# Performance work log

Measured on AMD Instinct MI355X. Metric: run time of the kernel, lower is better.

Reference implementation:

```python
import jax, jax.numpy as jnp
import numpy as np

N_NODES = 50000
N_EDGES = 1600000
IN_CH = 128
HID = 128
OUT_CH = 6
NUM_GRAPHS = 512


def _lin_params(key, fan_in, fan_out):
    k1, k2 = jax.random.split(key)
    bound = 1.0 / np.sqrt(fan_in)
    W = jax.random.uniform(k1, (fan_in, fan_out), minval=-bound, maxval=bound, dtype=jnp.float32)
    b = jax.random.uniform(k2, (fan_out,), minval=-bound, maxval=bound, dtype=jnp.float32)
    return W, b


def setup_inputs() -> dict:
    key = jax.random.key(0)
    ks = jax.random.split(key, 10)
    x = jax.random.normal(ks[0], (N_NODES, IN_CH), dtype=jnp.float32)
    edge_index = jax.random.randint(ks[1], (2, N_EDGES), 0, N_NODES, dtype=jnp.int64)
    batch = jnp.sort(jax.random.randint(ks[2], (N_NODES,), 0, NUM_GRAPHS, dtype=jnp.int64))
    W1a, b1a = _lin_params(ks[3], IN_CH, HID)
    W1b, b1b = _lin_params(ks[4], HID, HID)
    W2a, b2a = _lin_params(ks[5], HID, HID)
    W2b, b2b = _lin_params(ks[6], HID, HID)
    Wf1, bf1 = _lin_params(ks[7], HID, HID)
    Wf2, bf2 = _lin_params(ks[8], HID, OUT_CH)
    return {"x": x, "edge_index": edge_index, "batch": batch,
            "W1a": W1a, "b1a": b1a, "W1b": W1b, "b1b": b1b,
            "W2a": W2a, "b2a": b2a, "W2b": W2b, "b2b": b2b,
            "Wf1": Wf1, "bf1": bf1, "Wf2": Wf2, "bf2": bf2}


def _gin_conv(x, src, dst, Wa, ba, Wb, bb):
    # aggregate: sum of source-node features into target nodes (eps = 0)
    agg = jax.ops.segment_sum(x[src], dst, num_segments=N_NODES)
    h = x + agg  # (1 + eps) * x + sum_neighbors
    h = jax.nn.relu(h @ Wa + ba) @ Wb + bb  # 2-layer MLP (nn1/nn2)
    return h


def reference(x, edge_index, batch, W1a, b1a, W1b, b1b, W2a, b2a, W2b, b2b, Wf1, bf1, Wf2, bf2):
    src, dst = edge_index[0], edge_index[1]
    h = jax.nn.relu(_gin_conv(x, src, dst, W1a, b1a, W1b, b1b))
    h = jax.nn.relu(_gin_conv(h, src, dst, W2a, b2a, W2b, b2b))
    # global mean pool over graph ids
    sums = jax.ops.segment_sum(h, batch, num_segments=NUM_GRAPHS)  # [G, HID]
    counts = jax.ops.segment_sum(jnp.ones((h.shape[0],), h.dtype), batch, num_segments=NUM_GRAPHS)
    pooled = sums / jnp.maximum(counts, 1.0)[:, None]
    out = jax.nn.relu(pooled @ Wf1 + bf1) @ Wf2 + bf2  # [G, 6]
    return jax.nn.sigmoid(out)
```

## Files before the change

kernel.cpp:

```cpp
#include <hip/hip_runtime.h>

typedef unsigned short u16;
typedef unsigned int u32;

#define N_NODES 50000
#define N_EDGES 1600000
#define CH 128
#define CHW 64
#define NG 512
#define CAP 128
#define PAD 136
#define NBINS 196
#define BINCAP 12288
#define ECHUNK 6250

typedef __bf16 bf16x8 __attribute__((ext_vector_type(8)));
typedef float f32x4 __attribute__((ext_vector_type(4)));

#define OFF_DEG 0ull
#define OFF_BUCKET 200192ull
#define OFF_XB 13000192ull
#define OFF_HSUM 25800192ull
#define OFF_H1 38600192ull
#define OFF_POOL 51400192ull
#define OFF_GS 51662336ull
#define OFF_GE 51664384ull
#define OFF_WT 51666432ull
#define OFF_BC 51797504ull
#define OFF_WF1 51799552ull
#define OFF_BF1 51865088ull
#define OFF_WF2 51865600ull
#define OFF_BF2 51868672ull
#define OFF_BCUR 51868928ull

__device__ __forceinline__ float bflo(u32 v) { return __builtin_bit_cast(float, v << 16); }
__device__ __forceinline__ float bfhi(u32 v) { return __builtin_bit_cast(float, v & 0xffff0000u); }
__device__ __forceinline__ float bf2f(u16 v) { return __builtin_bit_cast(float, ((u32)v) << 16); }
__device__ __forceinline__ u16 f2bf(float f) {
    u32 x = __builtin_bit_cast(u32, f);
    x += 0x7fffu + ((x >> 16) & 1u);
    return (u16)(x >> 16);
}
__device__ __forceinline__ u32 pack2(float a, float b) {
    return (u32)f2bf(a) | ((u32)f2bf(b) << 16);
}
__device__ __forceinline__ bool probe_bf16(u32 w0) {
    u32 ex = (w0 >> 7) & 0xFFu;
    bool ok = ((w0 & 0x7FFFu) == 0u) || (ex >= 0x70u && ex <= 0x8Fu);
    return __popcll(__ballot(ok)) >= 48;
}
__device__ __forceinline__ float loadf(const void* p, int i, bool isbf) {
    return isbf ? bf2f(((const u16*)p)[i]) : ((const float*)p)[i];
}

__global__ __launch_bounds__(256) void prep_params(char* ws,
                                                   const void* W0, const void* W1,
                                                   const void* W2, const void* W3,
                                                   const void* b0, const void* b1,
                                                   const void* b2, const void* b3,
                                                   const void* Wf1, const void* bf1,
                                                   const void* Wf2, const void* bf2) {
    int lane = threadIdx.x & 63;
    bool isbf = probe_bf16(((const u32*)W0)[lane]);
    int idx = blockIdx.x * 256 + threadIdx.x;
    u16* Wt = (u16*)(ws + OFF_WT);
    float* bc = (float*)(ws + OFF_BC);
    float* Wf1c = (float*)(ws + OFF_WF1);
    float* bf1c = (float*)(ws + OFF_BF1);
    float* Wf2c = (float*)(ws + OFF_WF2);
    float* bf2c = (float*)(ws + OFF_BF2);
    if (idx < 65536) {
        int j = idx >> 14, r = idx & 16383;
        int n = r >> 7, k = r & 127;
        const void* src = (j == 0) ? W0 : (j == 1) ? W1 : (j == 2) ? W2 : W3;
        float v = loadf(src, k * 128 + n, isbf);
        Wt[idx] = f2bf(v);
    } else if (idx < 66048) {
        int r = idx - 65536, j = r >> 7, c = r & 127;
        const void* src = (j == 0) ? b0 : (j == 1) ? b1 : (j == 2) ? b2 : b3;
        bc[r] = loadf(src, c, isbf);
    } else if (idx < 82432) {
        Wf1c[idx - 66048] = loadf(Wf1, idx - 66048, isbf);
    } else if (idx < 82560) {
        bf1c[idx - 82432] = loadf(bf1, idx - 82432, isbf);
    } else if (idx < 83328) {
        Wf2c[idx - 82560] = loadf(Wf2, idx - 82560, isbf);
    } else if (idx < 83334) {
        bf2c[idx - 83328] = loadf(bf2, idx - 83328, isbf);
    }
}

__global__ __launch_bounds__(256) void cvt_x(const u32* __restrict__ x, u32* __restrict__ xb) {
    int lane = threadIdx.x & 63;
    bool isbf = probe_bf16(x[lane]);
    int i = blockIdx.x * 256 + threadIdx.x;
    if (i >= N_NODES * CHW) return;
    if (isbf) {
        xb[i] = x[i];
    } else {
        float2 v = ((const float2*)x)[i];
        xb[i] = pack2(v.x, v.y);
    }
}

__global__ __launch_bounds__(256) void edge_scatter(const int* __restrict__ ei,
                                                    int* __restrict__ binCursor,
                                                    u32* __restrict__ binned) {
    __shared__ u32 lhist[256];
    __shared__ u32 lbase[256];
    __shared__ u32 lcur[256];
    int tid = threadIdx.x, wg = blockIdx.x;
    int lane = tid & 63;
    u32 hiw = ((const u32*)ei)[2 * lane + 1];
    bool i64 = __popcll(__ballot(hiw == 0u)) >= 48;
    int e0 = wg * ECHUNK;
    lhist[tid] = 0; lcur[tid] = 0;
    __syncthreads();
    for (int e = e0 + tid; e < e0 + ECHUNK; e += 256) {
        int d = i64 ? ei[2 * N_EDGES + 2 * e] : ei[N_EDGES + e];
        atomicAdd(&lhist[d >> 8], 1u);
    }
    __syncthreads();
    u32 c = lhist[tid];
    if (c) lbase[tid] = (u32)atomicAdd(&binCursor[tid], (int)c);
    __syncthreads();
    for (int e = e0 + tid; e < e0 + ECHUNK; e += 256) {
        int s, d;
        if (i64) { s = ei[2 * e]; d = ei[2 * N_EDGES + 2 * e]; }
        else     { s = ei[e];     d = ei[N_EDGES + e]; }
        int b = d >> 8;
        u32 p = atomicAdd(&lcur[b], 1u);
        binned[(size_t)b * BINCAP + lbase[b] + p] = ((u32)d << 16) | (u32)s;
    }
}

__global__ __launch_bounds__(256) void fill_from_binned(const int* __restrict__ binCursor,
                                                        const u32* __restrict__ binned,
                                                        int* __restrict__ deg,
                                                        u16* __restrict__ bucket) {
    __shared__ u32 ldeg[256];
    int tid = threadIdx.x, b = blockIdx.x;
    int cnt = binCursor[b];
    ldeg[tid] = 0;
    __syncthreads();
    const u32* bp = binned + (size_t)b * BINCAP;
    for (int i = tid; i < cnt; i += 256) {
        u32 w = bp[i];
        u32 dl = (w >> 16) & 255u;
        u32 pos = atomicAdd(&ldeg[dl], 1u);
        if (pos < CAP) bucket[(size_t)(w >> 16) * CAP + pos] = (u16)(w & 0xFFFFu);
    }
    __syncthreads();
    int node = b * 256 + tid;
    if (node < N_NODES) deg[node] = (int)ldeg[tid];
}

__global__ __launch_bounds__(256) void agg_kernel(const u32* __restrict__ h,
                                                  const int* __restrict__ deg,
                                                  const u16* __restrict__ bucket,
                                                  u32* __restrict__ out) {
    int w = threadIdx.x >> 6, lane = threadIdx.x & 63;
    int node = blockIdx.x * 4 + w;
    if (node >= N_NODES) return;
    u32 self = h[(size_t)node * CHW + lane];
    float ax = bflo(self), ay = bfhi(self);
    int d = deg[node];
    d = d > CAP ? CAP : d;
    const u16* bk = bucket + (size_t)node * CAP;
    const u32* bkw = (const u32*)bk;
    int j = 0;
    for (; j + 8 <= d; j += 8) {
        u32 w0 = bkw[(j >> 1) + 0], w1 = bkw[(j >> 1) + 1];
        u32 w2 = bkw[(j >> 1) + 2], w3 = bkw[(j >> 1) + 3];
        u32 v0 = h[(size_t)(w0 & 0xFFFFu) * CHW + lane];
        u32 v1 = h[(size_t)(w0 >> 16) * CHW + lane];
        u32 v2 = h[(size_t)(w1 & 0xFFFFu) * CHW + lane];
        u32 v3 = h[(size_t)(w1 >> 16) * CHW + lane];
        u32 v4 = h[(size_t)(w2 & 0xFFFFu) * CHW + lane];
        u32 v5 = h[(size_t)(w2 >> 16) * CHW + lane];
        u32 v6 = h[(size_t)(w3 & 0xFFFFu) * CHW + lane];
        u32 v7 = h[(size_t)(w3 >> 16) * CHW + lane];
        ax += bflo(v0) + bflo(v1) + bflo(v2) + bflo(v3)
            + bflo(v4) + bflo(v5) + bflo(v6) + bflo(v7);
        ay += bfhi(v0) + bfhi(v1) + bfhi(v2) + bfhi(v3)
            + bfhi(v4) + bfhi(v5) + bfhi(v6) + bfhi(v7);
    }
    for (; j < d; ++j) {
        u32 v = h[(size_t)bk[j] * CHW + lane];
        ax += bflo(v);
        ay += bfhi(v);
    }
    out[(size_t)node * CHW + lane] = pack2(ax, ay);
}

__global__ __launch_bounds__(256) void mlp_kernel(const u16* __restrict__ in,
                                                  const u16* __restrict__ Wta,
                                                  const float* __restrict__ ba,
                                                  const u16* __restrict__ Wtb,
                                                  const float* __restrict__ bb,
                                                  u16* __restrict__ out,
                                                  int nrows) {
    __shared__ __align__(16) u16 Wlds[128 * PAD];
    __shared__ __align__(16) u16 tlds[64 * PAD];
    const int tid = threadIdx.x;
    const int w = tid >> 6;
    const int lane = tid & 63;
    const int n16 = lane & 15;
    const int quad = lane >> 4;
    const int row0 = blockIdx.x * 64 + w * 16;
    const bool active = row0 < nrows;

    {
        const uint4* wsrc = (const uint4*)Wta;
#pragma unroll
        for (int it = 0; it < 8; ++it) {
            int idx = tid + it * 256;
            int n = idx >> 4, c = idx & 15;
            *(uint4*)&Wlds[n * PAD + c * 8] = wsrc[idx];
        }
    }
    __syncthreads();

    f32x4 acc[8];
    bf16x8 afrag[4];
    if (active) {
        const u16* rowp = in + (size_t)(row0 + n16) * CH + quad * 8;
#pragma unroll
        for (int ks = 0; ks < 4; ++ks)
            afrag[ks] = *(const bf16x8*)(rowp + ks * 32);
#pragma unroll
        for (int ct = 0; ct < 8; ++ct) {
            f32x4 a = {0.f, 0.f, 0.f, 0.f};
#pragma unroll
            for (int ks = 0; ks < 4; ++ks) {
                bf16x8 b = *(const bf16x8*)&Wlds[(u32)(ct * 16 + n16) * PAD + ks * 32 + quad * 8];
                a = __builtin_amdgcn_mfma_f32_16x16x32_bf16(afrag[ks], b, a, 0, 0, 0);
            }
            acc[ct] = a;
        }
#pragma unroll
        for (int ct = 0; ct < 8; ++ct) {
            float bv = ba[ct * 16 + n16];
#pragma unroll
            for (int r = 0; r < 4; ++r) {
                float v = fmaxf(acc[ct][r] + bv, 0.f);
                tlds[(w * 16 + quad * 4 + r) * PAD + ct * 16 + n16] = f2bf(v);
            }
        }
    }
    __syncthreads();
    {
        const uint4* wsrc = (const uint4*)Wtb;
#pragma unroll
        for (int it = 0; it < 8; ++it) {
            int idx = tid + it * 256;
            int n = idx >> 4, c = idx & 15;
            *(uint4*)&Wlds[n * PAD + c * 8] = wsrc[idx];
        }
    }
    __syncthreads();

    if (active) {
#pragma unroll
        for (int ks = 0; ks < 4; ++ks)
            afrag[ks] = *(const bf16x8*)&tlds[(u32)(w * 16 + n16) * PAD + ks * 32 + quad * 8];
#pragma unroll
        for (int ct = 0; ct < 8; ++ct) {
            f32x4 a = {0.f, 0.f, 0.f, 0.f};
#pragma unroll
            for (int ks = 0; ks < 4; ++ks) {
                bf16x8 b = *(const bf16x8*)&Wlds[(u32)(ct * 16 + n16) * PAD + ks * 32 + quad * 8];
                a = __builtin_amdgcn_mfma_f32_16x16x32_bf16(afrag[ks], b, a, 0, 0, 0);
            }
            acc[ct] = a;
        }
#pragma unroll
        for (int ct = 0; ct < 8; ++ct) {
            float bv = bb[ct * 16 + n16];
#pragma unroll
            for (int r = 0; r < 4; ++r) {
                float v = fmaxf(acc[ct][r] + bv, 0.f);
                tlds[(w * 16 + quad * 4 + r) * PAD + ct * 16 + n16] = f2bf(v);
            }
        }
        u32* outw = (u32*)out;
        for (int r = 0; r < 16; ++r) {
            u32 v = *(const u32*)&tlds[(w * 16 + r) * PAD + lane * 2];
            outw[(size_t)(row0 + r) * CHW + lane] = v;
        }
    }
}

__global__ __launch_bounds__(256) void graph_bounds(const int* __restrict__ batch,
                                                    int* __restrict__ gstart,
                                                    int* __restrict__ gend) {
    int lane = threadIdx.x & 63;
    u32 hiw = ((const u32*)batch)[2 * (12500 + lane) + 1];
    bool i64 = __popcll(__ballot(hiw == 0u)) >= 48;
    int i = blockIdx.x * 256 + threadIdx.x;
    if (i >= N_NODES) return;
    int g = i64 ? batch[2 * i] : batch[i];
    atomicMin(&gstart[g], i);
    atomicMax(&gend[g], i + 1);
}

__global__ __launch_bounds__(256) void pool_kernel(const u32* __restrict__ h,
                                                   const int* __restrict__ gstart,
                                                   const int* __restrict__ gend,
                                                   float* __restrict__ pooled) {
    int w = threadIdx.x >> 6, lane = threadIdx.x & 63;
    int g = blockIdx.x * 4 + w;
    if (g >= NG) return;
    int s = gstart[g], e = gend[g];
    float ax = 0.f, ay = 0.f;
    if (s < e) {
        int i = s;
        for (; i + 4 <= e; i += 4) {
            u32 v0 = h[(size_t)(i + 0) * CHW + lane];
            u32 v1 = h[(size_t)(i + 1) * CHW + lane];
            u32 v2 = h[(size_t)(i + 2) * CHW + lane];
            u32 v3 = h[(size_t)(i + 3) * CHW + lane];
            ax += bflo(v0) + bflo(v1) + bflo(v2) + bflo(v3);
            ay += bfhi(v0) + bfhi(v1) + bfhi(v2) + bfhi(v3);
        }
        for (; i < e; ++i) {
            u32 v = h[(size_t)i * CHW + lane];
            ax += bflo(v);
            ay += bfhi(v);
        }
    }
    float inv = 1.f / (float)((s < e) ? (e - s) : 1);
    ((float2*)pooled)[(size_t)g * CHW + lane] = make_float2(ax * inv, ay * inv);
}

__global__ __launch_bounds__(256) void final_kernel(const float* __restrict__ pooled,
                                                    const float* __restrict__ Wf1,
                                                    const float* __restrict__ bf1,
                                                    const float* __restrict__ Wf2,
                                                    const float* __restrict__ bf2v,
                                                    float* __restrict__ out) {
    __shared__ float rowb[4][128];
    __shared__ float tb[4][128];
    int w = threadIdx.x >> 6, lane = threadIdx.x & 63;
    int g = blockIdx.x * 4 + w;
    float2 rv = ((const float2*)pooled)[(size_t)g * CHW + lane];
    rowb[w][2 * lane] = rv.x;
    rowb[w][2 * lane + 1] = rv.y;
    __syncthreads();
#pragma unroll
    for (int jj = 0; jj < 2; ++jj) {
        int j = lane + jj * 64;
        float a = bf1[j];
        for (int k = 0; k < 128; ++k) a += rowb[w][k] * Wf1[k * 128 + j];
        tb[w][j] = fmaxf(a, 0.f);
    }
    __syncthreads();
    if (lane < 6) {
        float a = bf2v[lane];
        for (int k = 0; k < 128; ++k) a += tb[w][k] * Wf2[k * 6 + lane];
        out[g * 6 + lane] = 1.f / (1.f + __expf(-a));
    }
}

extern "C" void kernel_launch(void* const* d_in, const int* in_sizes, int n_in,
                              void* d_out, int out_size, void* d_ws, size_t ws_size,
                              hipStream_t stream) {
    const u32* x = (const u32*)d_in[0];
    const int* ei = (const int*)d_in[1];
    const int* batch = (const int*)d_in[2];
    float* out = (float*)d_out;

    char* ws = (char*)d_ws;
    int* deg = (int*)(ws + OFF_DEG);
    u16* bucket = (u16*)(ws + OFF_BUCKET);
    u32* XB = (u32*)(ws + OFF_XB);
    u32* HSUM = (u32*)(ws + OFF_HSUM);
    u32* H1 = (u32*)(ws + OFF_H1);
    float* pooled = (float*)(ws + OFF_POOL);
    int* gstart = (int*)(ws + OFF_GS);
    int* gend = (int*)(ws + OFF_GE);
    u16* Wt = (u16*)(ws + OFF_WT);
    float* bc = (float*)(ws + OFF_BC);
    float* Wf1c = (float*)(ws + OFF_WF1);
    float* bf1c = (float*)(ws + OFF_BF1);
    float* Wf2c = (float*)(ws + OFF_WF2);
    float* bf2c = (float*)(ws + OFF_BF2);
    int* binCursor = (int*)(ws + OFF_BCUR);
    u32* binned = HSUM;

    hipMemsetAsync(binCursor, 0, 1024, stream);
    hipMemsetAsync(gstart, 0x7F, NG * 4, stream);
    hipMemsetAsync(gend, 0, NG * 4, stream);

    prep_params<<<326, 256, 0, stream>>>(ws,
        d_in[3], d_in[5], d_in[7], d_in[9],
        d_in[4], d_in[6], d_in[8], d_in[10],
        d_in[11], d_in[12], d_in[13], d_in[14]);
    cvt_x<<<(N_NODES * CHW) / 256, 256, 0, stream>>>(x, XB);
    edge_scatter<<<256, 256, 0, stream>>>(ei, binCursor, binned);
    fill_from_binned<<<NBINS, 256, 0, stream>>>(binCursor, binned, deg, bucket);
    graph_bounds<<<(N_NODES + 255) / 256, 256, 0, stream>>>(batch, gstart, gend);

    agg_kernel<<<(N_NODES + 3) / 4, 256, 0, stream>>>(XB, deg, bucket, HSUM);
    mlp_kernel<<<(N_NODES + 63) / 64, 256, 0, stream>>>((const u16*)HSUM, Wt, bc,
                                                        Wt + 16384, bc + 128, (u16*)H1, N_NODES);
    agg_kernel<<<(N_NODES + 3) / 4, 256, 0, stream>>>(H1, deg, bucket, HSUM);
    mlp_kernel<<<(N_NODES + 63) / 64, 256, 0, stream>>>((const u16*)HSUM, Wt + 32768, bc + 256,
                                                        Wt + 49152, bc + 384, (u16*)XB, N_NODES);
    pool_kernel<<<(NG + 3) / 4, 256, 0, stream>>>(XB, gstart, gend, pooled);
    final_kernel<<<NG / 4, 256, 0, stream>>>(pooled, Wf1c, bf1c, Wf2c, bf2c, out);
}
```

Before: 338.8 us.

## Split wavefront into four 16-lane groups gathering uint4 rows per neighbor

The aggregation kernel now has each wavefront split into four 16-lane subgroups. Each subgroup gathers a whole neighbor row with 16-byte loads, so four neighbors are in flight per instruction instead of one row gathered 4 bytes per lane. Partial sums are combined with cross-lane shuffles and written by one subgroup. Separately, the edge scatter launch doubles its block count and halves the per-block chunk, which depends on the unseen scatter kernel using ECHUNK consistently. The new layout adds shuffle-reduction overhead and carries more register accumulators.

Result: faster. 329.9 us (-2.6%).

```diff
diff --git a/kernel.cpp b/kernel.cpp
--- a/kernel.cpp
+++ b/kernel.cpp
@@ -12,7 +12,8 @@
 #define PAD 136
 #define NBINS 196
 #define BINCAP 12288
-#define ECHUNK 6250
+#define NSCAT 512
+#define ECHUNK 3125
 
 typedef __bf16 bf16x8 __attribute__((ext_vector_type(8)));
 typedef float f32x4 __attribute__((ext_vector_type(4)));
@@ -162,35 +163,73 @@
     int w = threadIdx.x >> 6, lane = threadIdx.x & 63;
     int node = blockIdx.x * 4 + w;
     if (node >= N_NODES) return;
-    u32 self = h[(size_t)node * CHW + lane];
-    float ax = bflo(self), ay = bfhi(self);
+    int sub = lane >> 4, q = lane & 15;
+    const uint4* h4 = (const uint4*)h;
+    float acc[8];
+    {
+        uint4 sv = make_uint4(0u, 0u, 0u, 0u);
+        if (sub == 0) sv = h4[(size_t)node * 16 + q];
+        acc[0] = bflo(sv.x); acc[1] = bfhi(sv.x);
+        acc[2] = bflo(sv.y); acc[3] = bfhi(sv.y);
+        acc[4] = bflo(sv.z); acc[5] = bfhi(sv.z);
+        acc[6] = bflo(sv.w); acc[7] = bfhi(sv.w);
+    }
     int d = deg[node];
     d = d > CAP ? CAP : d;
-    const u16* bk = bucket + (size_t)node * CAP;
-    const u32* bkw = (const u32*)bk;
+    const u32* bkw = (const u32*)(bucket + (size_t)node * CAP);
+    const u32 sh = (u32)(sub & 1) * 16u;
+    const int widx = sub >> 1;
     int j = 0;
-    for (; j + 8 <= d; j += 8) {
-        u32 w0 = bkw[(j >> 1) + 0], w1 = bkw[(j >> 1) + 1];
-        u32 w2 = bkw[(j >> 1) + 2], w3 = bkw[(j >> 1) + 3];
-        u32 v0 = h[(size_t)(w0 & 0xFFFFu) * CHW + lane];
-        u32 v1 = h[(size_t)(w0 >> 16) * CHW + lane];
-        u32 v2 = h[(size_t)(w1 & 0xFFFFu) * CHW + lane];
-        u32 v3 = h[(size_t)(w1 >> 16) * CHW + lane];
-        u32 v4 = h[(size_t)(w2 & 0xFFFFu) * CHW + lane];
-        u32 v5 = h[(size_t)(w2 >> 16) * CHW + lane];
-        u32 v6 = h[(size_t)(w3 & 0xFFFFu) * CHW + lane];
-        u32 v7 = h[(size_t)(w3 >> 16) * CHW + lane];
-        ax += bflo(v0) + bflo(v1) + bflo(v2) + bflo(v3)
-            + bflo(v4) + bflo(v5) + bflo(v6) + bflo(v7);
-        ay += bfhi(v0) + bfhi(v1) + bfhi(v2) + bfhi(v3)
-            + bfhi(v4) + bfhi(v5) + bfhi(v6) + bfhi(v7);
-    }
-    for (; j < d; ++j) {
-        u32 v = h[(size_t)bk[j] * CHW + lane];
-        ax += bflo(v);
-        ay += bfhi(v);
-    }
-    out[(size_t)node * CHW + lane] = pack2(ax, ay);
+    for (; j + 16 <= d; j += 16) {
+        int base = j >> 1;
+        u32 wd0 = bkw[base + widx];
+        u32 wd1 = bkw[base + 2 + widx];
+        u32 wd2 = bkw[base + 4 + widx];
+        u32 wd3 = bkw[base + 6 + widx];
+        uint4 v0 = h4[(size_t)((wd0 >> sh) & 0xFFFFu) * 16 + q];
+        uint4 v1 = h4[(size_t)((wd1 >> sh) & 0xFFFFu) * 16 + q];
+        uint4 v2 = h4[(size_t)((wd2 >> sh) & 0xFFFFu) * 16 + q];
+        uint4 v3 = h4[(size_t)((wd3 >> sh) & 0xFFFFu) * 16 + q];
+        acc[0] += bflo(v0.x) + bflo(v1.x) + bflo(v2.x) + bflo(v3.x);
+        acc[1] += bfhi(v0.x) + bfhi(v1.x) + bfhi(v2.x) + bfhi(v3.x);
+        acc[2] += bflo(v0.y) + bflo(v1.y) + bflo(v2.y) + bflo(v3.y);
+        acc[3] += bfhi(v0.y) + bfhi(v1.y) + bfhi(v2.y) + bfhi(v3.y);
+        acc[4] += bflo(v0.z) + bflo(v1.z) + bflo(v2.z) + bflo(v3.z);
+        acc[5] += bfhi(v0.z) + bfhi(v1.z) + bfhi(v2.z) + bfhi(v3.z);
+        acc[6] += bflo(v0.w) + bflo(v1.w) + bflo(v2.w) + bflo(v3.w);
+        acc[7] += bfhi(v0.w) + bfhi(v1.w) + bfhi(v2.w) + bfhi(v3.w);
+    }
+    for (; j + 4 <= d; j += 4) {
+        u32 wd = bkw[(j >> 1) + widx];
+        uint4 v = h4[(size_t)((wd >> sh) & 0xFFFFu) * 16 + q];
+        acc[0] += bflo(v.x); acc[1] += bfhi(v.x);
+        acc[2] += bflo(v.y); acc[3] += bfhi(v.y);
+        acc[4] += bflo(v.z); acc[5] += bfhi(v.z);
+        acc[6] += bflo(v.w); acc[7] += bfhi(v.w);
+    }
+    if (j + sub < d) {
+        int e = j + sub;
+        u32 wd = bkw[e >> 1];
+        u32 id = (wd >> ((u32)(e & 1) * 16u)) & 0xFFFFu;
+        uint4 v = h4[(size_t)id * 16 + q];
+        acc[0] += bflo(v.x); acc[1] += bfhi(v.x);
+        acc[2] += bflo(v.y); acc[3] += bfhi(v.y);
+        acc[4] += bflo(v.z); acc[5] += bfhi(v.z);
+        acc[6] += bflo(v.w); acc[7] += bfhi(v.w);
+    }
+#pragma unroll
+    for (int c = 0; c < 8; ++c) {
+        acc[c] += __shfl_xor(acc[c], 16, 64);
+        acc[c] += __shfl_xor(acc[c], 32, 64);
+    }
+    if (sub == 0) {
+        uint4 o;
+        o.x = pack2(acc[0], acc[1]);
+        o.y = pack2(acc[2], acc[3]);
+        o.z = pack2(acc[4], acc[5]);
+        o.w = pack2(acc[6], acc[7]);
+        ((uint4*)out)[(size_t)node * 16 + q] = o;
+    }
 }
 
 __global__ __launch_bounds__(256) void mlp_kernel(const u16* __restrict__ in,
@@ -397,7 +436,7 @@
         d_in[4], d_in[6], d_in[8], d_in[10],
         d_in[11], d_in[12], d_in[13], d_in[14]);
     cvt_x<<<(N_NODES * CHW) / 256, 256, 0, stream>>>(x, XB);
-    edge_scatter<<<256, 256, 0, stream>>>(ei, binCursor, binned);
+    edge_scatter<<<NSCAT, 256, 0, stream>>>(ei, binCursor, binned);
     fill_from_binned<<<NBINS, 256, 0, stream>>>(binCursor, binned, deg, bucket);
     graph_bounds<<<(N_NODES + 255) / 256, 256, 0, stream>>>(batch, gstart, gend);
 
```
